# Kernel optimization log

Hardware: AMD Instinct MI355X
Metric: run time of the kernel (lower is better)

The kernel has to match this reference:

```python
import jax, jax.numpy as jnp
import numpy as np

T, L, D, P, H = 1024, 32, 512, 512, 2048
EPS = 1e-5  # torch LayerNorm default eps


def _layer_norm(x, g, b):
    m = x.mean(axis=-1, keepdims=True)
    v = ((x - m) ** 2).mean(axis=-1, keepdims=True)
    return (x - m) * jax.lax.rsqrt(v + EPS) * g + b


def setup_inputs() -> dict:
    key = jax.random.key(0)
    ks = jax.random.split(key, 16)
    s = 0.02
    inp = {
        "base_prompts": jax.random.normal(ks[0], (T, L, D), jnp.float32),
        "new_prompt": jax.random.normal(ks[1], (L, D), jnp.float32),
        "task_embedding": jax.random.normal(ks[2], (D,), jnp.float32),
        # linear weights stored (in, out) so forward is x @ W + b
        "Wt": jax.random.normal(ks[3], (D, P), jnp.float32) * s,
        "bt": jnp.zeros((P,), jnp.float32),
        "Wq": jax.random.normal(ks[4], (D, P), jnp.float32) * s,
        "bq": jnp.zeros((P,), jnp.float32),
        "Wk": jax.random.normal(ks[5], (D, P), jnp.float32) * s,
        "bk": jnp.zeros((P,), jnp.float32),
        "Wv": jax.random.normal(ks[6], (D, P), jnp.float32) * s,
        "bv": jnp.zeros((P,), jnp.float32),
        "Wo": jax.random.normal(ks[7], (P, D), jnp.float32) * s,
        "bo": jnp.zeros((D,), jnp.float32),
        "Wa1": jax.random.normal(ks[8], (D, H), jnp.float32) * s,
        "ba1": jnp.zeros((H,), jnp.float32),
        "Wa2": jax.random.normal(ks[9], (H, D), jnp.float32) * s,
        "ba2": jnp.zeros((D,), jnp.float32),
        "g_in": jnp.ones((D,), jnp.float32),
        "b_in": jnp.zeros((D,), jnp.float32),
        "g_out": jnp.ones((D,), jnp.float32),
        "b_out": jnp.zeros((D,), jnp.float32),
    }
    return inp


def reference(base_prompts, new_prompt, task_embedding,
              Wt, bt, Wq, bq, Wk, bk, Wv, bv, Wo, bo,
              Wa1, ba1, Wa2, ba2, g_in, b_in, g_out, b_out):
    scale = 1.0 / np.sqrt(P).astype(np.float32)

    # --- task conditioning ---
    task_vec = jnp.tanh(task_embedding @ Wt + bt)                 # [P]
    key_repr = (base_prompts @ Wk + bk).mean(axis=1)              # [T,P]
    scores = (key_repr @ task_vec) * scale                        # [T]
    task_weights = jax.nn.softmax(scores)
    conditioned = base_prompts * (1.0 + task_weights[:, None, None])  # [T,L,D]

    query = new_prompt @ Wq + bq                                  # [L,P]
    keys = conditioned @ Wk + bk                                  # [T,L,P]
    values = conditioned @ Wv + bv                                # [T,L,P]

    # --- task-level attention ---
    pooled_q = query.mean(axis=0)                                 # [P]
    pooled_k = keys.mean(axis=1)                                  # [T,P]
    task_attn = jax.nn.softmax((pooled_k @ pooled_q) * scale)     # [T]
    task_weights = 0.5 * task_weights + 0.5 * task_attn
    task_weights = task_weights / jnp.maximum(task_weights.sum(), 1e-6)

    # --- enhanced mode: weighted pooling over tasks ---
    weighted_values = jnp.einsum('t,tlp->lp', task_weights, values)       # [L,P]
    weighted_keys = jnp.einsum('t,tlp->lp', task_weights, keys)           # [L,P]
    weighted_prompts = jnp.einsum('t,tld->ld', task_weights, conditioned) # [L,D]

    # --- feature-level attention ---
    feature_logits = (query @ weighted_keys.T) * scale            # [L,L]
    feature_attn = jax.nn.softmax(feature_logits, axis=-1)
    evolved_proj = feature_attn @ weighted_values                 # [L,P]

    evolved = evolved_proj @ Wo + bo                              # [L,D]
    evolved = _layer_norm(weighted_prompts + evolved, g_in, b_in)
    mlp = jax.nn.relu(evolved @ Wa1 + ba1) @ Wa2 + ba2
    aligned = _layer_norm(evolved + mlp, g_out, b_out)            # [L,D]

    aligned_prompts = jnp.broadcast_to(aligned, (T, L, D))        # stack of identical aligned prompts
    return aligned, aligned_prompts, task_weights, feature_attn
```

## Files before the change

### kernel.cpp

```cpp
#include <hip/hip_runtime.h>


static constexpr int T_ = 1024, L_ = 32, D_ = 512, P_ = 512, H_ = 2048;
static constexpr float SCALE = 0.04419417382415922f;
static constexpr float EPS_ = 1e-5f;

static constexpr int OFFO_AL = 0;
static constexpr int OFFO_AP = 16384;
static constexpr int OFFO_TW = 16384 + 16777216;
static constexpr int OFFO_FA = OFFO_TW + 1024;

static constexpr int OFF_SB      = 0;
static constexpr int OFF_AQP     = 524288;
static constexpr int OFF_QUERY   = 591872;
static constexpr int OFF_WKTV    = 608256;
static constexpr int OFF_WKPQ    = 608768;
static constexpr int OFF_SC      = 609280;
static constexpr int OFF_U       = 609344;
static constexpr int OFF_V       = 610368;
static constexpr int OFF_PART    = 611392;
static constexpr int OFF_WB      = 1135680;
static constexpr int OFF_AKVP    = 1152064;
static constexpr int OFF_EP2     = 1283136;
static constexpr int OFF_AH1P    = 1299520;
static constexpr int OFF_AOUTP   = 1561664;
static constexpr int OFF_AEVOP   = 1823808;
static constexpr int OFF_DUMMY   = 1954880;

__device__ __forceinline__ float wred64(float v) {
    #pragma unroll
    for (int off = 32; off > 0; off >>= 1) v += __shfl_down(v, off, 64);
    return v;
}
__device__ __forceinline__ float wmax64(float v) {
    #pragma unroll
    for (int off = 32; off > 0; off >>= 1) v = fmaxf(v, __shfl_down(v, off, 64));
    return v;
}
__device__ __forceinline__ float bsum512(float v, float* buf, int tid) {
    v = wred64(v);
    __syncthreads();
    if ((tid & 63) == 0) buf[tid >> 6] = v;
    __syncthreads();
    float s = 0.f;
    #pragma unroll
    for (int i = 0; i < 8; ++i) s += buf[i];
    return s;
}
__device__ __forceinline__ float bsum128(float v, float* buf, int tid) {
    v = wred64(v);
    __syncthreads();
    if ((tid & 63) == 0) buf[tid >> 6] = v;
    __syncthreads();
    return buf[0] + buf[1];
}
__device__ __forceinline__ float bmax128(float v, float* buf, int tid) {
    v = wmax64(v);
    __syncthreads();
    if ((tid & 63) == 0) buf[tid >> 6] = v;
    __syncthreads();
    return fmaxf(buf[0], buf[1]);
}

__global__ __launch_bounds__(512) void k_aq_sb(
    const float* __restrict__ base, const float* __restrict__ np_,
    const float* __restrict__ te, const float* __restrict__ Wq,
    const float* __restrict__ Wt, const float* __restrict__ Wk,
    const float* __restrict__ Wv, const float* __restrict__ Wo,
    const float* __restrict__ Wa1, const float* __restrict__ Wa2,
    float* __restrict__ ws)
{
    __shared__ __align__(16) float4 smem4[512];
    int blk = blockIdx.x, tid = threadIdx.x;
    if (blk < 176) {
        const float* src;
        int pw = blk;
        if (pw < 16)       src = Wo  + pw * 16384;
        else if (pw < 80)  src = Wa1 + (pw - 16) * 16384;
        else if (pw < 144) src = Wa2 + (pw - 80) * 16384;
        else if (pw < 160) src = Wk  + (pw - 144) * 16384;
        else               src = Wv  + (pw - 160) * 16384;
        const float4* s4 = (const float4*)src;
        float4 acc = make_float4(0.f, 0.f, 0.f, 0.f);
        #pragma unroll
        for (int i = 0; i < 8; ++i) {
            float4 v = s4[i * 512 + tid];
            acc.x += v.x; acc.y += v.y; acc.z += v.z; acc.w += v.w;
        }
        ws[OFF_DUMMY + pw * 512 + tid] = acc.x + acc.y + acc.z + acc.w;
    } else if (blk < 308) {
        float* sx = (float*)smem4;
        int b = (blk - 176) % 33, kc = (blk - 176) / 33;
        const float* x = (b < 32) ? (np_ + b * D_) : te;
        const float* W = (b < 32) ? Wq : Wt;
        if (tid < 128) sx[tid] = x[kc * 128 + tid];
        __syncthreads();
        float acc = 0.f;
        #pragma unroll 8
        for (int j = 0; j < 128; ++j) acc = fmaf(sx[j], W[(kc * 128 + j) * P_ + tid], acc);
        ws[OFF_AQP + (kc * 33 + b) * P_ + tid] = acc;
    } else {
        int t = blk - 308;
        const float4* bp = (const float4*)(base + (size_t)t * (L_ * D_));
        int d4 = tid & 127, lq = tid >> 7;
        float4 acc = make_float4(0.f, 0.f, 0.f, 0.f);
        #pragma unroll
        for (int i = 0; i < 8; ++i) {
            int l = i * 4 + lq;
            float4 v = bp[l * 128 + d4];
            acc.x += v.x; acc.y += v.y; acc.z += v.z; acc.w += v.w;
        }
        smem4[tid] = acc;
        __syncthreads();
        if (tid < 128) {
            float4 a = smem4[tid], b2 = smem4[tid + 128];
            float4 c = smem4[tid + 256], d2 = smem4[tid + 384];
            float4 r;
            r.x = a.x + b2.x + c.x + d2.x;
            r.y = a.y + b2.y + c.y + d2.y;
            r.z = a.z + b2.z + c.z + d2.z;
            r.w = a.w + b2.w + c.w + d2.w;
            ((float4*)(ws + OFF_SB + t * D_))[tid] = r;
        }
    }
}

__global__ __launch_bounds__(512) void k_prep(
    const float* __restrict__ Wk, const float* __restrict__ bk,
    const float* __restrict__ bq, const float* __restrict__ bt,
    float* __restrict__ ws)
{
    __shared__ __align__(16) float stv[512];
    __shared__ __align__(16) float spq[512];
    __shared__ float buf[8];
    int blk = blockIdx.x, tid = threadIdx.x;

    float a = 0.f;
    #pragma unroll
    for (int kc = 0; kc < 4; ++kc) a += ws[OFF_AQP + (kc * 33 + 32) * P_ + tid];
    stv[tid] = tanhf(a + bt[tid]);

    float b = 0.f;
    #pragma unroll 4
    for (int kc = 0; kc < 4; ++kc)
        for (int l = 0; l < 32; ++l) b += ws[OFF_AQP + (kc * 33 + l) * P_ + tid];
    spq[tid] = b * (1.f / 32.f) + bq[tid];

    if (blk < 32) {
        float q = bq[tid];
        #pragma unroll
        for (int kc = 0; kc < 4; ++kc) q += ws[OFF_AQP + (kc * 33 + blk) * P_ + tid];
        ws[OFF_QUERY + blk * P_ + tid] = q;
    }
    __syncthreads();

    int wv = tid >> 6, lane = tid & 63;
    int d = blk * 8 + wv;
    const float4* row = (const float4*)(Wk + d * P_);
    const float4* tv4 = (const float4*)stv;
    const float4* pq4 = (const float4*)spq;
    float4 r0 = row[lane * 2], r1 = row[lane * 2 + 1];
    float4 t0 = tv4[lane * 2], t1 = tv4[lane * 2 + 1];
    float4 q0 = pq4[lane * 2], q1 = pq4[lane * 2 + 1];
    float pa = r0.x * t0.x + r0.y * t0.y + r0.z * t0.z + r0.w * t0.w
             + r1.x * t1.x + r1.y * t1.y + r1.z * t1.z + r1.w * t1.w;
    float pb = r0.x * q0.x + r0.y * q0.y + r0.z * q0.z + r0.w * q0.w
             + r1.x * q1.x + r1.y * q1.y + r1.z * q1.z + r1.w * q1.w;
    pa = wred64(pa); pb = wred64(pb);
    if (lane == 0) { ws[OFF_WKTV + d] = pa; ws[OFF_WKPQ + d] = pb; }

    if (blk == 63) {
        float bkf = bk[tid];
        float s1 = bsum512(bkf * stv[tid], buf, tid);
        float s2 = bsum512(bkf * spq[tid], buf, tid);
        if (tid == 0) { ws[OFF_SC] = s1; ws[OFF_SC + 1] = s2; }
    }
}

__global__ __launch_bounds__(512) void k_uv(float* __restrict__ ws)
{
    __shared__ float buf[8];
    int t = blockIdx.x, tid = threadIdx.x;
    float sb = ws[OFF_SB + t * D_ + tid];
    float a = bsum512(sb * ws[OFF_WKTV + tid], buf, tid);
    float b = bsum512(sb * ws[OFF_WKPQ + tid], buf, tid);
    if (tid == 0) {
        ws[OFF_U + t] = a * (1.f / L_);
        ws[OFF_V + t] = b * (1.f / L_);
    }
}

__global__ __launch_bounds__(128) void k_part(
    const float* __restrict__ base, float* __restrict__ out_tw,
    float* __restrict__ ws)
{
    __shared__ float sC[1024];
    __shared__ float rbuf[2];
    int l = blockIdx.x, ch = blockIdx.y, tid = threadIdx.x;
    float bkt = ws[OFF_SC], bkq = ws[OFF_SC + 1];

    float u[8], v[8], s1[8], tw1[8], tw[8];
    #pragma unroll
    for (int i = 0; i < 8; ++i) {
        int t = i * 128 + tid;
        u[i] = ws[OFF_U + t];
        v[i] = ws[OFF_V + t];
    }
    float lmax = -1e30f;
    #pragma unroll
    for (int i = 0; i < 8; ++i) { s1[i] = (u[i] + bkt) * SCALE; lmax = fmaxf(lmax, s1[i]); }
    float gmax = bmax128(lmax, rbuf, tid);
    float ls = 0.f;
    #pragma unroll
    for (int i = 0; i < 8; ++i) { s1[i] = expf(s1[i] - gmax); ls += s1[i]; }
    float gs = bsum128(ls, rbuf, tid);
    #pragma unroll
    for (int i = 0; i < 8; ++i) tw1[i] = s1[i] / gs;
    lmax = -1e30f;
    #pragma unroll
    for (int i = 0; i < 8; ++i) {
        s1[i] = ((1.f + tw1[i]) * v[i] + bkq) * SCALE;
        lmax = fmaxf(lmax, s1[i]);
    }
    gmax = bmax128(lmax, rbuf, tid);
    ls = 0.f;
    #pragma unroll
    for (int i = 0; i < 8; ++i) { s1[i] = expf(s1[i] - gmax); ls += s1[i]; }
    gs = bsum128(ls, rbuf, tid);
    float lsum = 0.f;
    #pragma unroll
    for (int i = 0; i < 8; ++i) {
        tw[i] = 0.5f * tw1[i] + 0.5f * (s1[i] / gs);
        lsum += tw[i];
    }
    float S = bsum128(lsum, rbuf, tid);
    S = fmaxf(S, 1e-6f);
    #pragma unroll
    for (int i = 0; i < 8; ++i) {
        int t = i * 128 + tid;
        float twn = tw[i] / S;
        sC[t] = twn * (1.f + tw1[i]);
        if (l == 0 && ch == 0) out_tw[t] = twn;
    }
    __syncthreads();

    float4 acc = make_float4(0.f, 0.f, 0.f, 0.f);
    for (int i = 0; i < 32; ++i) {
        int t = ch * 32 + i;
        float c = sC[t];
        float4 bv4 = ((const float4*)(base + ((size_t)t * L_ + l) * D_))[tid];
        acc.x = fmaf(c, bv4.x, acc.x);
        acc.y = fmaf(c, bv4.y, acc.y);
        acc.z = fmaf(c, bv4.z, acc.z);
        acc.w = fmaf(c, bv4.w, acc.w);
    }
    ((float4*)(ws + OFF_PART + (ch * 32 + l) * D_))[tid] = acc;
}

__global__ __launch_bounds__(512) void k_kv(
    const float* __restrict__ Wk, const float* __restrict__ Wv,
    float* __restrict__ ws)
{
    __shared__ float part[512];
    __shared__ float sx[128];
    int blk = blockIdx.x, tid = threadIdx.x;
    int l = blk & 31, sel = (blk >> 5) & 1, kc = blk >> 6;
    int p = tid & 127, c = tid >> 7;
    float s = 0.f;
    #pragma unroll
    for (int ch = c; ch < 32; ch += 4)
        s += ws[OFF_PART + (ch * 32 + l) * D_ + kc * 128 + p];
    part[tid] = s;
    __syncthreads();
    if (tid < 128) {
        float w = part[tid] + part[tid + 128] + part[tid + 256] + part[tid + 384];
        sx[tid] = w;
        if (sel == 0) ws[OFF_WB + l * D_ + kc * 128 + tid] = w;
    }
    __syncthreads();
    const float* W = sel ? Wv : Wk;
    float acc = 0.f;
    #pragma unroll 8
    for (int j = 0; j < 128; ++j) acc = fmaf(sx[j], W[(kc * 128 + j) * P_ + tid], acc);
    ws[OFF_AKVP + ((kc * 2 + sel) * 32 + l) * P_ + tid] = acc;
}

__global__ __launch_bounds__(512) void k_attn(
    const float* __restrict__ bk, const float* __restrict__ bv,
    float* __restrict__ out_fa, float* __restrict__ ws)
{
    __shared__ __align__(16) float sq[512];
    __shared__ float slg[32];
    __shared__ float sfa[32];
    int l = blockIdx.x, tid = threadIdx.x, wv = tid >> 6, lane = tid & 63;
    sq[tid] = ws[OFF_QUERY + l * P_ + tid];
    __syncthreads();

    const float4* sq4 = (const float4*)sq;
    const float4* bk4 = (const float4*)bk;
    float4 q0 = sq4[lane * 2], q1 = sq4[lane * 2 + 1];
    float4 kb0 = bk4[lane * 2], kb1 = bk4[lane * 2 + 1];
    #pragma unroll
    for (int gi = 0; gi < 4; ++gi) {
        int g = wv * 4 + gi;
        float4 A = kb0, B = kb1;
        #pragma unroll
        for (int kc = 0; kc < 4; ++kc) {
            const float4* kr = (const float4*)(ws + OFF_AKVP + ((kc * 2) * 32 + g) * P_);
            float4 a = kr[lane * 2], b = kr[lane * 2 + 1];
            A.x += a.x; A.y += a.y; A.z += a.z; A.w += a.w;
            B.x += b.x; B.y += b.y; B.z += b.z; B.w += b.w;
        }
        float sdot = A.x * q0.x + A.y * q0.y + A.z * q0.z + A.w * q0.w
                   + B.x * q1.x + B.y * q1.y + B.z * q1.z + B.w * q1.w;
        sdot = wred64(sdot);
        if (lane == 0) slg[g] = sdot * SCALE;
    }
    __syncthreads();
    if (tid < 32) {
        float mx = -1e30f;
        for (int i = 0; i < 32; ++i) mx = fmaxf(mx, slg[i]);
        float Ssm = 0.f;
        for (int i = 0; i < 32; ++i) Ssm += expf(slg[i] - mx);
        float f = expf(slg[tid] - mx) / Ssm;
        sfa[tid] = f;
        out_fa[l * 32 + tid] = f;
    }
    __syncthreads();

    float bvp = bv[tid];
    float acc = 0.f;
    #pragma unroll 4
    for (int j = 0; j < 32; ++j) {
        float vs = ws[OFF_AKVP + ((0 * 2 + 1) * 32 + j) * P_ + tid]
                 + ws[OFF_AKVP + ((1 * 2 + 1) * 32 + j) * P_ + tid]
                 + ws[OFF_AKVP + ((2 * 2 + 1) * 32 + j) * P_ + tid]
                 + ws[OFF_AKVP + ((3 * 2 + 1) * 32 + j) * P_ + tid];
        acc = fmaf(sfa[j], vs + bvp, acc);
    }
    ws[OFF_EP2 + l * P_ + tid] = acc;
}

__global__ __launch_bounds__(512) void k_evo(
    const float* __restrict__ Wo, float* __restrict__ ws)
{
    __shared__ float sx[64];
    int l = blockIdx.x, kc = blockIdx.y, tid = threadIdx.x;
    if (tid < 64) sx[tid] = ws[OFF_EP2 + l * P_ + kc * 64 + tid];
    __syncthreads();
    float acc = 0.f;
    #pragma unroll 8
    for (int j = 0; j < 64; ++j) acc = fmaf(sx[j], Wo[(kc * 64 + j) * D_ + tid], acc);
    ws[OFF_AEVOP + (kc * 32 + l) * D_ + tid] = acc;
}

__global__ __launch_bounds__(512) void k_mlp1(
    const float* __restrict__ Wa1, const float* __restrict__ bo,
    const float* __restrict__ g_in, const float* __restrict__ b_in,
    float* __restrict__ ws)
{
    __shared__ float sevo[512];
    __shared__ float buf[8];
    int blk = blockIdx.x, tid = threadIdx.x;
    int l = blk & 31, hc = (blk >> 5) & 3, kc = blk >> 7;
    float x = ws[OFF_WB + l * D_ + tid] + bo[tid];
    #pragma unroll
    for (int k2 = 0; k2 < 8; ++k2) x += ws[OFF_AEVOP + (k2 * 32 + l) * D_ + tid];
    float mean = bsum512(x, buf, tid) * (1.f / D_);
    float dx = x - mean;
    float var = bsum512(dx * dx, buf, tid) * (1.f / D_);
    sevo[tid] = dx * rsqrtf(var + EPS_) * g_in[tid] + b_in[tid];
    __syncthreads();
    int h = hc * 512 + tid;
    float acc = 0.f;
    #pragma unroll 8
    for (int j = 0; j < 128; ++j) acc = fmaf(sevo[kc * 128 + j], Wa1[(kc * 128 + j) * H_ + h], acc);
    ws[OFF_AH1P + (kc * 32 + l) * H_ + h] = acc;
}

__global__ __launch_bounds__(512) void k_mlp2(
    const float* __restrict__ Wa2, const float* __restrict__ ba1,
    float* __restrict__ ws)
{
    __shared__ float sh[128];
    int blk = blockIdx.x, tid = threadIdx.x;
    int l = blk & 31, kc = blk >> 5;
    if (tid < 128) {
        int h = kc * 128 + tid;
        float a = ba1[h];
        #pragma unroll
        for (int k4 = 0; k4 < 4; ++k4) a += ws[OFF_AH1P + (k4 * 32 + l) * H_ + h];
        sh[tid] = fmaxf(a, 0.f);
    }
    __syncthreads();
    float acc = 0.f;
    #pragma unroll 8
    for (int j = 0; j < 128; ++j) acc = fmaf(sh[j], Wa2[(kc * 128 + j) * D_ + tid], acc);
    ws[OFF_AOUTP + (kc * 32 + l) * D_ + tid] = acc;
}

__global__ __launch_bounds__(512) void k_lnout(
    const float* __restrict__ bo, const float* __restrict__ g_in,
    const float* __restrict__ b_in, const float* __restrict__ ba2,
    const float* __restrict__ g_out, const float* __restrict__ b_out,
    float* __restrict__ out_al, float* __restrict__ ws)
{
    __shared__ float buf[8];
    int l = blockIdx.x, tid = threadIdx.x;
    float x = ws[OFF_WB + l * D_ + tid] + bo[tid];
    #pragma unroll
    for (int k2 = 0; k2 < 8; ++k2) x += ws[OFF_AEVOP + (k2 * 32 + l) * D_ + tid];
    float mean = bsum512(x, buf, tid) * (1.f / D_);
    float dx = x - mean;
    float var = bsum512(dx * dx, buf, tid) * (1.f / D_);
    float evo = dx * rsqrtf(var + EPS_) * g_in[tid] + b_in[tid];
    float x2 = evo + ba2[tid];
    #pragma unroll
    for (int kc = 0; kc < 16; ++kc) x2 += ws[OFF_AOUTP + (kc * 32 + l) * D_ + tid];
    float mean2 = bsum512(x2, buf, tid) * (1.f / D_);
    float dx2 = x2 - mean2;
    float var2 = bsum512(dx2 * dx2, buf, tid) * (1.f / D_);
    out_al[l * D_ + tid] = dx2 * rsqrtf(var2 + EPS_) * g_out[tid] + b_out[tid];
}

__global__ __launch_bounds__(256) void k_bcast(float* __restrict__ out) {
    const float4* src = (const float4*)out;
    float4* dst = (float4*)(out + OFFO_AP);
    int idx = blockIdx.x * 256 + threadIdx.x;
    #pragma unroll
    for (int k = 0; k < 4; ++k) {
        int v = idx + k * 1048576;
        dst[v] = src[v & 4095];
    }
}

extern "C" void kernel_launch(void* const* d_in, const int* in_sizes, int n_in,
                              void* d_out, int out_size, void* d_ws, size_t ws_size,
                              hipStream_t stream) {
    const float* base = (const float*)d_in[0];
    const float* np   = (const float*)d_in[1];
    const float* te   = (const float*)d_in[2];
    const float* Wt   = (const float*)d_in[3];
    const float* bt   = (const float*)d_in[4];
    const float* Wq   = (const float*)d_in[5];
    const float* bq   = (const float*)d_in[6];
    const float* Wk   = (const float*)d_in[7];
    const float* bk   = (const float*)d_in[8];
    const float* Wv   = (const float*)d_in[9];
    const float* bv   = (const float*)d_in[10];
    const float* Wo   = (const float*)d_in[11];
    const float* bo   = (const float*)d_in[12];
    const float* Wa1  = (const float*)d_in[13];
    const float* ba1  = (const float*)d_in[14];
    const float* Wa2  = (const float*)d_in[15];
    const float* ba2  = (const float*)d_in[16];
    const float* g_in = (const float*)d_in[17];
    const float* b_in = (const float*)d_in[18];
    const float* g_out= (const float*)d_in[19];
    const float* b_out= (const float*)d_in[20];
    float* out = (float*)d_out;
    float* ws = out + OFFO_AP;

    hipLaunchKernelGGL(k_aq_sb, dim3(1332),    dim3(512), 0, stream,
                       base, np, te, Wq, Wt, Wk, Wv, Wo, Wa1, Wa2, ws);
    hipLaunchKernelGGL(k_prep,  dim3(64),      dim3(512), 0, stream, Wk, bk, bq, bt, ws);
    hipLaunchKernelGGL(k_uv,    dim3(1024),    dim3(512), 0, stream, ws);
    hipLaunchKernelGGL(k_part,  dim3(32, 32),  dim3(128), 0, stream, base, out + OFFO_TW, ws);
    hipLaunchKernelGGL(k_kv,    dim3(256),     dim3(512), 0, stream, Wk, Wv, ws);
    hipLaunchKernelGGL(k_attn,  dim3(32),      dim3(512), 0, stream, bk, bv, out + OFFO_FA, ws);
    hipLaunchKernelGGL(k_evo,   dim3(32, 8),   dim3(512), 0, stream, Wo, ws);
    hipLaunchKernelGGL(k_mlp1,  dim3(512),     dim3(512), 0, stream, Wa1, bo, g_in, b_in, ws);
    hipLaunchKernelGGL(k_mlp2,  dim3(512),     dim3(512), 0, stream, Wa2, ba1, ws);
    hipLaunchKernelGGL(k_lnout, dim3(32),      dim3(512), 0, stream,
                       bo, g_in, b_in, ba2, g_out, b_out, out + OFFO_AL, ws);
    hipLaunchKernelGGL(k_bcast, dim3(4096),    dim3(256), 0, stream, out);
}
```

Measured before the change: 258.4 us.

## Split attention into parallel logits, fuse softmax-V with Wo, fuse broadcast into LayerNorm

The 32-block attention kernel becomes a 256-block logits kernel plus a kernel that recomputes the softmax per block, does the value-weighted sum for a 64-wide slice, and applies Wo directly. The separate broadcast kernel is folded into the final LayerNorm, which now runs on a 32x32 grid and writes the replicated rows from shared memory. Scratch moves from the output buffer to the dedicated workspace. This cuts launches and raises parallelism in small serial stages, at the cost of redundant softmax and LayerNorm work per block.

```diff
diff --git a/kernel.cpp b/kernel.cpp
--- a/kernel.cpp
+++ b/kernel.cpp
@@ -21,11 +21,11 @@
 static constexpr int OFF_PART    = 611392;
 static constexpr int OFF_WB      = 1135680;
 static constexpr int OFF_AKVP    = 1152064;
-static constexpr int OFF_EP2     = 1283136;
-static constexpr int OFF_AH1P    = 1299520;
-static constexpr int OFF_AOUTP   = 1561664;
-static constexpr int OFF_AEVOP   = 1823808;
-static constexpr int OFF_DUMMY   = 1954880;
+static constexpr int OFF_LG      = 1283136;
+static constexpr int OFF_AH1P    = 1284160;
+static constexpr int OFF_AOUTP   = 1546304;
+static constexpr int OFF_AEVOP   = 1808448;
+static constexpr int OFF_DUMMY   = 1939520;
 
 __device__ __forceinline__ float wred64(float v) {
     #pragma unroll
@@ -285,73 +285,80 @@
     ws[OFF_AKVP + ((kc * 2 + sel) * 32 + l) * P_ + tid] = acc;
 }
 
-__global__ __launch_bounds__(512) void k_attn(
-    const float* __restrict__ bk, const float* __restrict__ bv,
-    float* __restrict__ out_fa, float* __restrict__ ws)
+__global__ __launch_bounds__(512) void k_logits(
+    const float* __restrict__ bk, float* __restrict__ ws)
 {
     __shared__ __align__(16) float sq[512];
-    __shared__ float slg[32];
-    __shared__ float sfa[32];
-    int l = blockIdx.x, tid = threadIdx.x, wv = tid >> 6, lane = tid & 63;
+    int l = blockIdx.x, gc = blockIdx.y, tid = threadIdx.x;
+    int wv = tid >> 6, lane = tid & 63;
     sq[tid] = ws[OFF_QUERY + l * P_ + tid];
     __syncthreads();
-
     const float4* sq4 = (const float4*)sq;
     const float4* bk4 = (const float4*)bk;
     float4 q0 = sq4[lane * 2], q1 = sq4[lane * 2 + 1];
-    float4 kb0 = bk4[lane * 2], kb1 = bk4[lane * 2 + 1];
-    #pragma unroll
-    for (int gi = 0; gi < 4; ++gi) {
-        int g = wv * 4 + gi;
-        float4 A = kb0, B = kb1;
-        #pragma unroll
-        for (int kc = 0; kc < 4; ++kc) {
-            const float4* kr = (const float4*)(ws + OFF_AKVP + ((kc * 2) * 32 + g) * P_);
-            float4 a = kr[lane * 2], b = kr[lane * 2 + 1];
-            A.x += a.x; A.y += a.y; A.z += a.z; A.w += a.w;
-            B.x += b.x; B.y += b.y; B.z += b.z; B.w += b.w;
-        }
-        float sdot = A.x * q0.x + A.y * q0.y + A.z * q0.z + A.w * q0.w
-                   + B.x * q1.x + B.y * q1.y + B.z * q1.z + B.w * q1.w;
-        sdot = wred64(sdot);
-        if (lane == 0) slg[g] = sdot * SCALE;
-    }
+    float4 A = bk4[lane * 2], B = bk4[lane * 2 + 1];
+    int g = gc * 4 + wv;
+    #pragma unroll
+    for (int kc = 0; kc < 4; ++kc) {
+        const float4* kr = (const float4*)(ws + OFF_AKVP + ((kc * 2) * 32 + g) * P_);
+        float4 a = kr[lane * 2], b = kr[lane * 2 + 1];
+        A.x += a.x; A.y += a.y; A.z += a.z; A.w += a.w;
+        B.x += b.x; B.y += b.y; B.z += b.z; B.w += b.w;
+    }
+    float sdot = A.x * q0.x + A.y * q0.y + A.z * q0.z + A.w * q0.w
+               + B.x * q1.x + B.y * q1.y + B.z * q1.z + B.w * q1.w;
+    sdot = wred64(sdot);
+    if (lane == 0) ws[OFF_LG + l * 32 + g] = sdot * SCALE;
+}
+
+__global__ __launch_bounds__(512) void k_evoEP(
+    const float* __restrict__ bv, const float* __restrict__ Wo,
+    float* __restrict__ out_fa, float* __restrict__ ws)
+{
+    __shared__ float slg[32];
+    __shared__ float sfa[32];
+    __shared__ float pe[8][64];
+    __shared__ float sx[64];
+    int l = blockIdx.x, kc = blockIdx.y, tid = threadIdx.x;
+    if (tid < 32) slg[tid] = ws[OFF_LG + l * 32 + tid];
     __syncthreads();
     if (tid < 32) {
         float mx = -1e30f;
         for (int i = 0; i < 32; ++i) mx = fmaxf(mx, slg[i]);
-        float Ssm = 0.f;
-        for (int i = 0; i < 32; ++i) Ssm += expf(slg[i] - mx);
-        float f = expf(slg[tid] - mx) / Ssm;
+        float S = 0.f;
+        for (int i = 0; i < 32; ++i) S += expf(slg[i] - mx);
+        float f = expf(slg[tid] - mx) / S;
         sfa[tid] = f;
-        out_fa[l * 32 + tid] = f;
-    }
-    __syncthreads();
-
-    float bvp = bv[tid];
+        if (kc == 0) out_fa[l * 32 + tid] = f;
+    }
+    __syncthreads();
+
+    int p = tid & 63, jg = tid >> 6;
+    float bvp = bv[kc * 64 + p];
     float acc = 0.f;
-    #pragma unroll 4
-    for (int j = 0; j < 32; ++j) {
-        float vs = ws[OFF_AKVP + ((0 * 2 + 1) * 32 + j) * P_ + tid]
-                 + ws[OFF_AKVP + ((1 * 2 + 1) * 32 + j) * P_ + tid]
-                 + ws[OFF_AKVP + ((2 * 2 + 1) * 32 + j) * P_ + tid]
-                 + ws[OFF_AKVP + ((3 * 2 + 1) * 32 + j) * P_ + tid];
+    #pragma unroll
+    for (int jj = 0; jj < 4; ++jj) {
+        int j = jg * 4 + jj;
+        float vs = ws[OFF_AKVP + (1 * 32 + j) * P_ + kc * 64 + p]
+                 + ws[OFF_AKVP + (3 * 32 + j) * P_ + kc * 64 + p]
+                 + ws[OFF_AKVP + (5 * 32 + j) * P_ + kc * 64 + p]
+                 + ws[OFF_AKVP + (7 * 32 + j) * P_ + kc * 64 + p];
         acc = fmaf(sfa[j], vs + bvp, acc);
     }
-    ws[OFF_EP2 + l * P_ + tid] = acc;
-}
-
-__global__ __launch_bounds__(512) void k_evo(
-    const float* __restrict__ Wo, float* __restrict__ ws)
-{
-    __shared__ float sx[64];
-    int l = blockIdx.x, kc = blockIdx.y, tid = threadIdx.x;
-    if (tid < 64) sx[tid] = ws[OFF_EP2 + l * P_ + kc * 64 + tid];
-    __syncthreads();
-    float acc = 0.f;
+    pe[jg][p] = acc;
+    __syncthreads();
+    if (tid < 64) {
+        float s = 0.f;
+        #pragma unroll
+        for (int i = 0; i < 8; ++i) s += pe[i][tid];
+        sx[tid] = s;
+    }
+    __syncthreads();
+
+    float a2 = 0.f;
     #pragma unroll 8
-    for (int j = 0; j < 64; ++j) acc = fmaf(sx[j], Wo[(kc * 64 + j) * D_ + tid], acc);
-    ws[OFF_AEVOP + (kc * 32 + l) * D_ + tid] = acc;
+    for (int j = 0; j < 64; ++j) a2 = fmaf(sx[j], Wo[(kc * 64 + j) * D_ + tid], a2);
+    ws[OFF_AEVOP + (kc * 32 + l) * D_ + tid] = a2;
 }
 
 __global__ __launch_bounds__(512) void k_mlp1(
@@ -399,14 +406,15 @@
     ws[OFF_AOUTP + (kc * 32 + l) * D_ + tid] = acc;
 }
 
-__global__ __launch_bounds__(512) void k_lnout(
+__global__ __launch_bounds__(512) void k_lnbcast(
     const float* __restrict__ bo, const float* __restrict__ g_in,
     const float* __restrict__ b_in, const float* __restrict__ ba2,
     const float* __restrict__ g_out, const float* __restrict__ b_out,
-    float* __restrict__ out_al, float* __restrict__ ws)
+    float* __restrict__ out, float* __restrict__ ws)
 {
     __shared__ float buf[8];
-    int l = blockIdx.x, tid = threadIdx.x;
+    __shared__ __align__(16) float sal[512];
+    int l = blockIdx.x, tc = blockIdx.y, tid = threadIdx.x;
     float x = ws[OFF_WB + l * D_ + tid] + bo[tid];
     #pragma unroll
     for (int k2 = 0; k2 < 8; ++k2) x += ws[OFF_AEVOP + (k2 * 32 + l) * D_ + tid];
@@ -420,17 +428,16 @@
     float mean2 = bsum512(x2, buf, tid) * (1.f / D_);
     float dx2 = x2 - mean2;
     float var2 = bsum512(dx2 * dx2, buf, tid) * (1.f / D_);
-    out_al[l * D_ + tid] = dx2 * rsqrtf(var2 + EPS_) * g_out[tid] + b_out[tid];
-}
-
-__global__ __launch_bounds__(256) void k_bcast(float* __restrict__ out) {
-    const float4* src = (const float4*)out;
-    float4* dst = (float4*)(out + OFFO_AP);
-    int idx = blockIdx.x * 256 + threadIdx.x;
-    #pragma unroll
-    for (int k = 0; k < 4; ++k) {
-        int v = idx + k * 1048576;
-        dst[v] = src[v & 4095];
+    float a = dx2 * rsqrtf(var2 + EPS_) * g_out[tid] + b_out[tid];
+    if (tc == 0) out[OFFO_AL + l * D_ + tid] = a;
+    sal[tid] = a;
+    __syncthreads();
+    float4 v = ((const float4*)sal)[tid & 127];
+    int row = tid >> 7;
+    #pragma unroll
+    for (int pass = 0; pass < 8; ++pass) {
+        int t = tc * 32 + pass * 4 + row;
+        ((float4*)(out + OFFO_AP + (size_t)t * (L_ * D_) + l * D_))[tid & 127] = v;
     }
 }
 
@@ -459,19 +466,18 @@
     const float* g_out= (const float*)d_in[19];
     const float* b_out= (const float*)d_in[20];
     float* out = (float*)d_out;
-    float* ws = out + OFFO_AP;
-
-    hipLaunchKernelGGL(k_aq_sb, dim3(1332),    dim3(512), 0, stream,
+    float* ws = (float*)d_ws;
+
+    hipLaunchKernelGGL(k_aq_sb,   dim3(1332),   dim3(512), 0, stream,
                        base, np, te, Wq, Wt, Wk, Wv, Wo, Wa1, Wa2, ws);
-    hipLaunchKernelGGL(k_prep,  dim3(64),      dim3(512), 0, stream, Wk, bk, bq, bt, ws);
-    hipLaunchKernelGGL(k_uv,    dim3(1024),    dim3(512), 0, stream, ws);
-    hipLaunchKernelGGL(k_part,  dim3(32, 32),  dim3(128), 0, stream, base, out + OFFO_TW, ws);
-    hipLaunchKernelGGL(k_kv,    dim3(256),     dim3(512), 0, stream, Wk, Wv, ws);
-    hipLaunchKernelGGL(k_attn,  dim3(32),      dim3(512), 0, stream, bk, bv, out + OFFO_FA, ws);
-    hipLaunchKernelGGL(k_evo,   dim3(32, 8),   dim3(512), 0, stream, Wo, ws);
-    hipLaunchKernelGGL(k_mlp1,  dim3(512),     dim3(512), 0, stream, Wa1, bo, g_in, b_in, ws);
-    hipLaunchKernelGGL(k_mlp2,  dim3(512),     dim3(512), 0, stream, Wa2, ba1, ws);
-    hipLaunchKernelGGL(k_lnout, dim3(32),      dim3(512), 0, stream,
-                       bo, g_in, b_in, ba2, g_out, b_out, out + OFFO_AL, ws);
-    hipLaunchKernelGGL(k_bcast, dim3(4096),    dim3(256), 0, stream, out);
-}
+    hipLaunchKernelGGL(k_prep,    dim3(64),     dim3(512), 0, stream, Wk, bk, bq, bt, ws);
+    hipLaunchKernelGGL(k_uv,      dim3(1024),   dim3(512), 0, stream, ws);
+    hipLaunchKernelGGL(k_part,    dim3(32, 32), dim3(128), 0, stream, base, out + OFFO_TW, ws);
+    hipLaunchKernelGGL(k_kv,      dim3(256),    dim3(512), 0, stream, Wk, Wv, ws);
+    hipLaunchKernelGGL(k_logits,  dim3(32, 8),  dim3(512), 0, stream, bk, ws);
+    hipLaunchKernelGGL(k_evoEP,   dim3(32, 8),  dim3(512), 0, stream, bv, Wo, out + OFFO_FA, ws);
+    hipLaunchKernelGGL(k_mlp1,    dim3(512),    dim3(512), 0, stream, Wa1, bo, g_in, b_in, ws);
+    hipLaunchKernelGGL(k_mlp2,    dim3(512),    dim3(512), 0, stream, Wa2, ba1, ws);
+    hipLaunchKernelGGL(k_lnbcast, dim3(32, 32), dim3(512), 0, stream,
+                       bo, g_in, b_in, ba2, g_out, b_out, out, ws);
+}
```

Measured after the change: 256.9 us. Within noise of the previous version (-0.6%).
